# Performance work log

Measured on AMD Instinct MI355X. Metric: run time of the kernel, lower is better.

## Reference

```python
import jax, jax.numpy as jnp
import numpy as np

KERNEL = (3, 3)
STRIDE = (1, 1)


def setup_inputs() -> dict:
    key = jax.random.key(0)
    k1, k2 = jax.random.split(key)
    x = jax.random.normal(k1, (8, 32, 32, 64), dtype=jnp.float32)
    # unshared weights: [H_out, W_out, C_in*kh*kw, C_out]
    lc_params = jax.random.normal(k2, (30, 30, 64 * 3 * 3, 64), dtype=jnp.float32) * 0.02
    return {"x": x, "lc_params": lc_params}


def reference(x, lc_params):
    # im2col patch extraction; feature dim ordered [C_in, kh, kw] (C slowest),
    # exactly matching the layout the original param tensor is trained against.
    x_unf = jax.lax.conv_general_dilated_patches(
        lhs=x,
        filter_shape=KERNEL,
        window_strides=STRIDE,
        padding='VALID',
        dimension_numbers=('NHWC', 'HWIO', 'NHWC'),
    )  # [B, H_out, W_out, C*kh*kw]
    # per-location contraction; same math as (x_unf[..., None] * lc_params).sum(3)
    # but lowered as a batched matmul instead of materializing [B,H,W,K,O].
    out = jnp.einsum('bhwk,hwko->bhwo', x_unf, lc_params)
    return out
```

## Files before the change

kernel.cpp:

```cpp
#include <hip/hip_runtime.h>


#define HO 30
#define WO 30
#define HI 32
#define WI 32
#define CI 64
#define CO 64
#define BATCH 8
#define KTOT 576

__global__ __launch_bounds__(256) void lc_kernel(const float* __restrict__ x,
                                                 const float* __restrict__ wgt,
                                                 float* __restrict__ out) {
    const int hw = blockIdx.x;
    const int h  = hw / WO;
    const int w  = hw - h * WO;
    const int tid = threadIdx.x;

    __shared__ float smem[8192];
    float* xs = smem;

    #pragma unroll
    for (int it = 0; it < 18; ++it) {
        int idx = it * 256 + tid;
        int c  = idx & 63;
        int t  = idx >> 6;
        int b  = t / 9;
        int r  = t - b * 9;
        int kh = r / 3;
        int kw = r - kh * 3;
        float v = x[((b * HI + h + kh) * WI + (w + kw)) * CI + c];
        xs[b * KTOT + c * 9 + kh * 3 + kw] = v;
    }
    __syncthreads();

    const int o4 = tid & 15;
    const int kg = tid >> 4;

    const float4* w4 = reinterpret_cast<const float4*>(
                           wgt + (size_t)hw * KTOT * CO) + o4;

    float4 acc[BATCH];
    #pragma unroll
    for (int b = 0; b < BATCH; ++b) acc[b] = make_float4(0.f, 0.f, 0.f, 0.f);

    const int k0base = kg * 36;
    for (int i = 0; i < 9; ++i) {
        const int k0 = k0base + 4 * i;
        float4 w0 = w4[(k0 + 0) * 16];
        float4 w1 = w4[(k0 + 1) * 16];
        float4 w2 = w4[(k0 + 2) * 16];
        float4 w3 = w4[(k0 + 3) * 16];
        #pragma unroll
        for (int b = 0; b < BATCH; ++b) {
            float4 xv = *reinterpret_cast<const float4*>(&xs[b * KTOT + k0]);
            acc[b].x = fmaf(xv.x, w0.x, acc[b].x);
            acc[b].y = fmaf(xv.x, w0.y, acc[b].y);
            acc[b].z = fmaf(xv.x, w0.z, acc[b].z);
            acc[b].w = fmaf(xv.x, w0.w, acc[b].w);
            acc[b].x = fmaf(xv.y, w1.x, acc[b].x);
            acc[b].y = fmaf(xv.y, w1.y, acc[b].y);
            acc[b].z = fmaf(xv.y, w1.z, acc[b].z);
            acc[b].w = fmaf(xv.y, w1.w, acc[b].w);
            acc[b].x = fmaf(xv.z, w2.x, acc[b].x);
            acc[b].y = fmaf(xv.z, w2.y, acc[b].y);
            acc[b].z = fmaf(xv.z, w2.z, acc[b].z);
            acc[b].w = fmaf(xv.z, w2.w, acc[b].w);
            acc[b].x = fmaf(xv.w, w3.x, acc[b].x);
            acc[b].y = fmaf(xv.w, w3.y, acc[b].y);
            acc[b].z = fmaf(xv.w, w3.z, acc[b].z);
            acc[b].w = fmaf(xv.w, w3.w, acc[b].w);
        }
    }

    __syncthreads();
    float4* p4 = reinterpret_cast<float4*>(smem);
    #pragma unroll
    for (int b = 0; b < BATCH; ++b) p4[(kg * BATCH + b) * 16 + o4] = acc[b];
    __syncthreads();

    if (tid < 128) {
        int b   = tid >> 4;
        int oo4 = tid & 15;
        float4 s = make_float4(0.f, 0.f, 0.f, 0.f);
        #pragma unroll
        for (int kgi = 0; kgi < 16; ++kgi) {
            float4 v = p4[(kgi * BATCH + b) * 16 + oo4];
            s.x += v.x; s.y += v.y; s.z += v.z; s.w += v.w;
        }
        float* dst = out + (((size_t)b * HO + h) * WO + w) * CO + oo4 * 4;
        *reinterpret_cast<float4*>(dst) = s;
    }
}

extern "C" void kernel_launch(void* const* d_in, const int* in_sizes, int n_in,
                              void* d_out, int out_size, void* d_ws, size_t ws_size,
                              hipStream_t stream) {
    const float* x   = (const float*)d_in[0];
    const float* wgt = (const float*)d_in[1];
    float* out       = (float*)d_out;
    lc_kernel<<<dim3(HO * WO), dim3(256), 0, stream>>>(x, wgt, out);
}
```

Before: 194.8 us.

## Prefetch weights before x staging, double-buffer loads, reduce via wave shuffles

Weight loads for the first two k-chunks are issued before the input patch is staged into shared memory, and the k loop is fully unrolled with two register buffers so the next chunk's loads overlap the current FMAs. Weight loads use nontemporal hints because each weight element is read once. The cross-thread reduction now uses xor shuffles within each wave plus a small shared buffer across four waves, replacing the 16-way shared-memory reduction. Register pressure goes up with the double buffering.

```diff
diff --git a/kernel.cpp b/kernel.cpp
--- a/kernel.cpp
+++ b/kernel.cpp
@@ -10,16 +10,34 @@
 #define BATCH 8
 #define KTOT 576
 
+typedef float f32x4 __attribute__((ext_vector_type(4)));
+
 __global__ __launch_bounds__(256) void lc_kernel(const float* __restrict__ x,
                                                  const float* __restrict__ wgt,
                                                  float* __restrict__ out) {
     const int hw = blockIdx.x;
     const int h  = hw / WO;
     const int w  = hw - h * WO;
-    const int tid = threadIdx.x;
+    const int tid  = threadIdx.x;
+    const int lane = tid & 63;
+    const int wv   = tid >> 6;
+    const int o4   = tid & 15;
+    const int kg   = tid >> 4;
+    const int kb   = kg * 36;
 
-    __shared__ float smem[8192];
-    float* xs = smem;
+    __shared__ __align__(16) float xs[BATCH * KTOT];
+    __shared__ f32x4 pbuf[3][BATCH][16];
+
+    const f32x4* w4 = reinterpret_cast<const f32x4*>(
+                          wgt + (size_t)hw * KTOT * CO) + o4;
+
+    f32x4 wb0[4], wb1[4];
+    #pragma unroll
+    for (int j = 0; j < 4; ++j)
+        wb0[j] = __builtin_nontemporal_load(&w4[(kb + 0 + j) * 16]);
+    #pragma unroll
+    for (int j = 0; j < 4; ++j)
+        wb1[j] = __builtin_nontemporal_load(&w4[(kb + 4 + j) * 16]);
 
     #pragma unroll
     for (int it = 0; it < 18; ++it) {
@@ -35,62 +53,67 @@
     }
     __syncthreads();
 
-    const int o4 = tid & 15;
-    const int kg = tid >> 4;
+    f32x4 acc[BATCH];
+    #pragma unroll
+    for (int b = 0; b < BATCH; ++b) acc[b] = (f32x4)0.f;
 
-    const float4* w4 = reinterpret_cast<const float4*>(
-                           wgt + (size_t)hw * KTOT * CO) + o4;
-
-    float4 acc[BATCH];
-    #pragma unroll
-    for (int b = 0; b < BATCH; ++b) acc[b] = make_float4(0.f, 0.f, 0.f, 0.f);
-
-    const int k0base = kg * 36;
-    for (int i = 0; i < 9; ++i) {
-        const int k0 = k0base + 4 * i;
-        float4 w0 = w4[(k0 + 0) * 16];
-        float4 w1 = w4[(k0 + 1) * 16];
-        float4 w2 = w4[(k0 + 2) * 16];
-        float4 w3 = w4[(k0 + 3) * 16];
+    auto consume = [&](f32x4 (&cw)[4], int k0) {
         #pragma unroll
         for (int b = 0; b < BATCH; ++b) {
-            float4 xv = *reinterpret_cast<const float4*>(&xs[b * KTOT + k0]);
-            acc[b].x = fmaf(xv.x, w0.x, acc[b].x);
-            acc[b].y = fmaf(xv.x, w0.y, acc[b].y);
-            acc[b].z = fmaf(xv.x, w0.z, acc[b].z);
-            acc[b].w = fmaf(xv.x, w0.w, acc[b].w);
-            acc[b].x = fmaf(xv.y, w1.x, acc[b].x);
-            acc[b].y = fmaf(xv.y, w1.y, acc[b].y);
-            acc[b].z = fmaf(xv.y, w1.z, acc[b].z);
-            acc[b].w = fmaf(xv.y, w1.w, acc[b].w);
-            acc[b].x = fmaf(xv.z, w2.x, acc[b].x);
-            acc[b].y = fmaf(xv.z, w2.y, acc[b].y);
-            acc[b].z = fmaf(xv.z, w2.z, acc[b].z);
-            acc[b].w = fmaf(xv.z, w2.w, acc[b].w);
-            acc[b].x = fmaf(xv.w, w3.x, acc[b].x);
-            acc[b].y = fmaf(xv.w, w3.y, acc[b].y);
-            acc[b].z = fmaf(xv.w, w3.z, acc[b].z);
-            acc[b].w = fmaf(xv.w, w3.w, acc[b].w);
+            f32x4 xv = *reinterpret_cast<const f32x4*>(&xs[b * KTOT + k0]);
+            #pragma unroll
+            for (int j = 0; j < 4; ++j) {
+                acc[b][0] = fmaf(xv[j], cw[j][0], acc[b][0]);
+                acc[b][1] = fmaf(xv[j], cw[j][1], acc[b][1]);
+                acc[b][2] = fmaf(xv[j], cw[j][2], acc[b][2]);
+                acc[b][3] = fmaf(xv[j], cw[j][3], acc[b][3]);
+            }
+        }
+    };
+
+    #define RELOAD(buf, I)                                                   \
+        {                                                                    \
+            _Pragma("unroll")                                                \
+            for (int j = 0; j < 4; ++j)                                      \
+                buf[j] = __builtin_nontemporal_load(&w4[(kb + 4*(I) + j) * 16]); \
+        }
+
+    consume(wb0, kb + 0);  RELOAD(wb0, 2)
+    consume(wb1, kb + 4);  RELOAD(wb1, 3)
+    consume(wb0, kb + 8);  RELOAD(wb0, 4)
+    consume(wb1, kb + 12); RELOAD(wb1, 5)
+    consume(wb0, kb + 16); RELOAD(wb0, 6)
+    consume(wb1, kb + 20); RELOAD(wb1, 7)
+    consume(wb0, kb + 24); RELOAD(wb0, 8)
+    consume(wb1, kb + 28);
+    consume(wb0, kb + 32);
+    #undef RELOAD
+
+    #pragma unroll
+    for (int b = 0; b < BATCH; ++b) {
+        #pragma unroll
+        for (int m = 16; m < 64; m <<= 1) {
+            acc[b][0] += __shfl_xor(acc[b][0], m, 64);
+            acc[b][1] += __shfl_xor(acc[b][1], m, 64);
+            acc[b][2] += __shfl_xor(acc[b][2], m, 64);
+            acc[b][3] += __shfl_xor(acc[b][3], m, 64);
         }
     }
 
+    if (wv > 0 && lane < 16) {
+        #pragma unroll
+        for (int b = 0; b < BATCH; ++b) pbuf[wv - 1][b][o4] = acc[b];
+    }
     __syncthreads();
-    float4* p4 = reinterpret_cast<float4*>(smem);
-    #pragma unroll
-    for (int b = 0; b < BATCH; ++b) p4[(kg * BATCH + b) * 16 + o4] = acc[b];
-    __syncthreads();
-
-    if (tid < 128) {
-        int b   = tid >> 4;
-        int oo4 = tid & 15;
-        float4 s = make_float4(0.f, 0.f, 0.f, 0.f);
+    if (wv == 0 && lane < 16) {
         #pragma unroll
-        for (int kgi = 0; kgi < 16; ++kgi) {
-            float4 v = p4[(kgi * BATCH + b) * 16 + oo4];
-            s.x += v.x; s.y += v.y; s.z += v.z; s.w += v.w;
+        for (int b = 0; b < BATCH; ++b) {
+            f32x4 s = acc[b];
+            #pragma unroll
+            for (int p = 0; p < 3; ++p) s += pbuf[p][b][o4];
+            float* dst = out + (((size_t)b * HO + h) * WO + w) * CO + o4 * 4;
+            *reinterpret_cast<f32x4*>(dst) = s;
         }
-        float* dst = out + (((size_t)b * HO + h) * WO + w) * CO + oo4 * 4;
-        *reinterpret_cast<float4*>(dst) = s;
     }
 }
 
```

Measured after the change: 183.4 us. 5.9% less time.
